# Optimization experiments

Hardware: AMD Instinct MI355X
Metric: run time of the kernel (lower is better)

## Reference

```python
import jax, jax.numpy as jnp
import numpy as np

K = 5          # top-k constant (init k)
EPSILON = 1.0  # smoothing constant (init epsilon)
N_SAMPLE = 8   # noise samples (init n_sample)


def setup_inputs() -> dict:
    key = jax.random.key(0)
    k1, k2, k3 = jax.random.split(key, 3)
    n, d, m = 64, 100000, N_SAMPLE
    s = jax.random.normal(k1, (n, d), dtype=jnp.float32)
    y = jax.random.randint(k2, (n,), 0, d, dtype=jnp.int32)
    # In torch this noise is drawn inside forward(); we materialize it as an
    # input for a deterministic reference.  shape (n_batch, d, n_sample)
    Z = jax.random.normal(k3, (n, d, m), dtype=jnp.float32)
    return {"s": s, "y": y, "Z": Z}


def reference(s, y, Z):
    """Balanced noised top-k (calibrated hinge) loss of Garcin et al., ICML'22.

    loss_i = relu(1 + smoothed_kth_max(s_i excluding class y_i) - s_{i,y_i})
    where smoothed_kth_max(v) = E_Z[ kth-largest(v + eps*Z) ] estimated with
    n_sample Gaussian draws.  Returns the batch mean.
    """
    n, d = s.shape
    # Exclude the ground-truth score from the top-k pool (s^{\y}); -inf entries
    # can never enter the top-k since k < d, so this is equivalent to dropping
    # the column while keeping a rectangular, jit-friendly shape.
    is_y = jnp.arange(d)[None, :] == y[:, None]          # (n, d)
    s_ny = jnp.where(is_y, -jnp.inf, s)                  # (n, d)
    # Perturbed scores: (n, m, d)
    pert = s_ny[:, None, :] + EPSILON * jnp.swapaxes(Z, 1, 2)
    topk_vals = jax.lax.top_k(pert, K)[0]                # (n, m, K)
    kth_smooth = topk_vals[..., K - 1].mean(axis=1)      # (n,) Monte-Carlo E[kth max]
    s_y = jnp.take_along_axis(s, y[:, None].astype(jnp.int32), axis=1)[:, 0]
    loss = jnp.maximum(1.0 + kth_smooth - s_y, 0.0)
    return loss.mean()
```

## Files before the change

### kernel.cpp

```cpp
#include <hip/hip_runtime.h>
#include <math.h>


#define KTOP 5
#define MSAMP 8
#define TPB 256
#define NCHUNKS 32

__device__ __forceinline__ void topk_insert_bl(float (&v)[KTOP], float x) {
    float n0 = __builtin_amdgcn_fmed3f(x, v[0], v[1]);
    float n1 = __builtin_amdgcn_fmed3f(x, v[1], v[2]);
    float n2 = __builtin_amdgcn_fmed3f(x, v[2], v[3]);
    float n3 = __builtin_amdgcn_fmed3f(x, v[3], v[4]);
    float n4 = fmaxf(v[4], x);
    v[0] = n0; v[1] = n1; v[2] = n2; v[3] = n3; v[4] = n4;
}

__global__ __launch_bounds__(TPB) void topk_partial(
    const float* __restrict__ s, const int* __restrict__ y,
    const float* __restrict__ Z, float* __restrict__ cand,
    int d, int nchunks, int chunk)
{
    const int i = blockIdx.x / nchunks;
    const int c = blockIdx.x % nchunks;
    const int e0 = c * chunk;
    const int e1 = min(e0 + chunk, d);
    const int yi = y[i];

    const int t = threadIdx.x;
    const int j = t & 7;
    const int eofs = t >> 3;

    const float* __restrict__ srow = s + (size_t)i * d;
    const float* __restrict__ zrow = Z + (size_t)i * d * MSAMP;

    float v[KTOP];
    #pragma unroll
    for (int q = 0; q < KTOP; ++q) v[q] = -INFINITY;

    #pragma unroll 8
    for (int e = e0 + eofs; e < e1; e += 32) {
        float sv = srow[e];
        float z  = zrow[(size_t)e * MSAMP + j];
        float x  = (e == yi) ? -INFINITY : (sv + z);
        topk_insert_bl(v, x);
    }

    #pragma unroll
    for (int off = 8; off <= 32; off <<= 1) {
        float o[KTOP];
        #pragma unroll
        for (int q = 0; q < KTOP; ++q) o[q] = __shfl_xor(v[q], off, 64);
        #pragma unroll
        for (int q = 0; q < KTOP; ++q) topk_insert_bl(v, o[q]);
    }

    __shared__ float lds[TPB / 64][MSAMP][KTOP];
    const int wave = t >> 6;
    const int lane = t & 63;
    if (lane < MSAMP) {
        #pragma unroll
        for (int q = 0; q < KTOP; ++q) lds[wave][lane][q] = v[q];
    }
    __syncthreads();

    if (t < MSAMP) {
        float f[KTOP];
        #pragma unroll
        for (int q = 0; q < KTOP; ++q) f[q] = lds[0][t][q];
        #pragma unroll
        for (int w = 1; w < TPB / 64; ++w)
            #pragma unroll
            for (int q = 0; q < KTOP; ++q) topk_insert_bl(f, lds[w][t][q]);
        float* out = cand + (((size_t)i * nchunks + c) * MSAMP + t) * KTOP;
        #pragma unroll
        for (int q = 0; q < KTOP; ++q) out[q] = f[q];
    }
}

__global__ __launch_bounds__(TPB) void row_loss(
    const float* __restrict__ s, const int* __restrict__ y,
    const float* __restrict__ cand, float* __restrict__ rloss,
    int d, int nchunks)
{
    const int i = blockIdx.x;
    const int t = threadIdx.x;
    const int j = t & 7;
    const int wave = t >> 6;
    const int lane = t & 63;

    float v[KTOP];
    #pragma unroll
    for (int q = 0; q < KTOP; ++q) v[q] = -INFINITY;

    for (int c = t >> 3; c < nchunks; c += TPB / MSAMP) {
        const float* p = cand + (((size_t)i * nchunks + c) * MSAMP + j) * KTOP;
        #pragma unroll
        for (int q = 0; q < KTOP; ++q) topk_insert_bl(v, p[q]);
    }

    #pragma unroll
    for (int off = 8; off <= 32; off <<= 1) {
        float o[KTOP];
        #pragma unroll
        for (int q = 0; q < KTOP; ++q) o[q] = __shfl_xor(v[q], off, 64);
        #pragma unroll
        for (int q = 0; q < KTOP; ++q) topk_insert_bl(v, o[q]);
    }

    __shared__ float lds[TPB / 64][MSAMP][KTOP];
    __shared__ float kth_j[MSAMP];
    if (lane < MSAMP) {
        #pragma unroll
        for (int q = 0; q < KTOP; ++q) lds[wave][lane][q] = v[q];
    }
    __syncthreads();

    if (t < MSAMP) {
        float f[KTOP];
        #pragma unroll
        for (int q = 0; q < KTOP; ++q) f[q] = lds[0][t][q];
        #pragma unroll
        for (int w = 1; w < TPB / 64; ++w)
            #pragma unroll
            for (int q = 0; q < KTOP; ++q) topk_insert_bl(f, lds[w][t][q]);
        kth_j[t] = f[0];
    }
    __syncthreads();

    if (t == 0) {
        float sum = 0.0f;
        #pragma unroll
        for (int jj = 0; jj < MSAMP; ++jj) sum += kth_j[jj];
        float kth_smooth = sum * (1.0f / (float)MSAMP);
        float sy = s[(size_t)i * d + y[i]];
        rloss[i] = fmaxf(1.0f + kth_smooth - sy, 0.0f);
    }
}

__global__ __launch_bounds__(64) void mean_loss(
    const float* __restrict__ rloss, float* __restrict__ out, int n)
{
    const int t = threadIdx.x;
    float x = (t < n) ? rloss[t] : 0.0f;
    #pragma unroll
    for (int off = 32; off >= 1; off >>= 1) x += __shfl_xor(x, off, 64);
    if (t == 0) out[0] = x / (float)n;
}

extern "C" void kernel_launch(void* const* d_in, const int* in_sizes, int n_in,
                              void* d_out, int out_size, void* d_ws, size_t ws_size,
                              hipStream_t stream) {
    const float* s = (const float*)d_in[0];
    const int*   y = (const int*)d_in[1];
    const float* Z = (const float*)d_in[2];
    float* out = (float*)d_out;

    const int n = in_sizes[1];
    const int d = in_sizes[0] / n;

    int nchunks = NCHUNKS;
    while (nchunks > 1 &&
           (size_t)n * nchunks * MSAMP * KTOP * sizeof(float) + n * sizeof(float)
               > ws_size) {
        nchunks >>= 1;
    }
    int chunk = (d + nchunks - 1) / nchunks;
    chunk = (chunk + 31) & ~31;
    float* cand  = (float*)d_ws;
    float* rloss = cand + (size_t)n * nchunks * MSAMP * KTOP;

    hipLaunchKernelGGL(topk_partial, dim3(n * nchunks), dim3(TPB), 0, stream,
                       s, y, Z, cand, d, nchunks, chunk);
    hipLaunchKernelGGL(row_loss, dim3(n), dim3(TPB), 0, stream,
                       s, y, cand, rloss, d, nchunks);
    hipLaunchKernelGGL(mean_loss, dim3(1), dim3(64), 0, stream,
                       rloss, out, n);
}
```

Baseline: 44.42 us.

## Vectorize Z loads as float4 with four independent top-k lists per thread

Each thread now handles half of an element's eight samples, reading them as one float4 and keeping four independent top-k register lists instead of one. The s value is loaded once per four samples rather than once per sample, and the butterfly reduction is extended across more lanes. The goal is wider memory transactions and more instruction-level parallelism in the bandwidth-bound scan over Z. The cost is higher register pressure and a longer shuffle-merge phase, and chunk sizes are now rounded to multiples of 128.

New measurement: 46.94 us. +5.7%, slower.

```diff
diff --git a/kernel.cpp b/kernel.cpp
--- a/kernel.cpp
+++ b/kernel.cpp
@@ -28,39 +28,49 @@
     const int yi = y[i];
 
     const int t = threadIdx.x;
-    const int j = t & 7;
-    const int eofs = t >> 3;
+    const int h = t & 1;
+    const int eofs = t >> 1;
 
     const float* __restrict__ srow = s + (size_t)i * d;
     const float* __restrict__ zrow = Z + (size_t)i * d * MSAMP;
 
-    float v[KTOP];
+    float v[4][KTOP];
     #pragma unroll
-    for (int q = 0; q < KTOP; ++q) v[q] = -INFINITY;
+    for (int l = 0; l < 4; ++l)
+        #pragma unroll
+        for (int q = 0; q < KTOP; ++q) v[l][q] = -INFINITY;
 
-    #pragma unroll 8
-    for (int e = e0 + eofs; e < e1; e += 32) {
+    #pragma unroll 4
+    for (int e = e0 + eofs; e < e1; e += TPB / 2) {
         float sv = srow[e];
-        float z  = zrow[(size_t)e * MSAMP + j];
-        float x  = (e == yi) ? -INFINITY : (sv + z);
-        topk_insert_bl(v, x);
+        const float4 z = *(const float4*)(zrow + (size_t)e * MSAMP + h * 4);
+        sv = (e == yi) ? -INFINITY : sv;
+        topk_insert_bl(v[0], sv + z.x);
+        topk_insert_bl(v[1], sv + z.y);
+        topk_insert_bl(v[2], sv + z.z);
+        topk_insert_bl(v[3], sv + z.w);
     }
 
     #pragma unroll
-    for (int off = 8; off <= 32; off <<= 1) {
-        float o[KTOP];
+    for (int off = 2; off <= 32; off <<= 1) {
         #pragma unroll
-        for (int q = 0; q < KTOP; ++q) o[q] = __shfl_xor(v[q], off, 64);
-        #pragma unroll
-        for (int q = 0; q < KTOP; ++q) topk_insert_bl(v, o[q]);
+        for (int l = 0; l < 4; ++l) {
+            float o[KTOP];
+            #pragma unroll
+            for (int q = 0; q < KTOP; ++q) o[q] = __shfl_xor(v[l][q], off, 64);
+            #pragma unroll
+            for (int q = 0; q < KTOP; ++q) topk_insert_bl(v[l], o[q]);
+        }
     }
 
     __shared__ float lds[TPB / 64][MSAMP][KTOP];
     const int wave = t >> 6;
     const int lane = t & 63;
-    if (lane < MSAMP) {
+    if (lane < 2) {
         #pragma unroll
-        for (int q = 0; q < KTOP; ++q) lds[wave][lane][q] = v[q];
+        for (int l = 0; l < 4; ++l)
+            #pragma unroll
+            for (int q = 0; q < KTOP; ++q) lds[wave][lane * 4 + l][q] = v[l][q];
     }
     __syncthreads();
 
@@ -166,7 +176,7 @@
         nchunks >>= 1;
     }
     int chunk = (d + nchunks - 1) / nchunks;
-    chunk = (chunk + 31) & ~31;
+    chunk = (chunk + 127) & ~127;
     float* cand  = (float*)d_ws;
     float* rloss = cand + (size_t)n * nchunks * MSAMP * KTOP;
 
```
